# Kernel tuning notes

Measured on AMD Instinct MI355X. Metric: run time of the kernel, lower is better.

Reference implementation:

```python
import jax, jax.numpy as jnp
import numpy as np
from jax.scipy.linalg import expm

B, T, N_IN, N_HID, N_OUT = 8192, 2048, 2, 10, 10


def setup_inputs() -> dict:
    key = jax.random.key(0)
    k0, k1, k2, k3, k4 = jax.random.split(key, 5)
    inputs = jax.random.normal(k0, (B, T, N_IN), dtype=jnp.float32)
    # skew-symmetric seed for the orthogonal recurrent kernel (expm parametrization)
    A = jax.random.normal(k1, (N_HID, N_HID), dtype=jnp.float32) * 0.1
    # input_kernel: nn.Linear(n_inputs, n_hidden, bias=False) -> weight [H, D_in]
    W_in = jax.random.normal(k2, (N_HID, N_IN), dtype=jnp.float32) / np.sqrt(N_IN)
    # modrelu bias, initialized uniform(-0.01, 0.01) as in exprnn
    b_mod = jax.random.uniform(k3, (N_HID,), jnp.float32, -0.01, 0.01)
    # final nn.Linear(n_hidden, n_outputs)
    lin_W = jax.random.normal(k4, (N_OUT, N_HID), dtype=jnp.float32) / np.sqrt(N_HID)
    lin_b = jnp.zeros((N_OUT,), jnp.float32)
    return {"inputs": inputs, "A": A, "W_in": W_in, "b_mod": b_mod,
            "lin_W": lin_W, "lin_b": lin_b}


def _modrelu(z, b):
    # modrelu(z) = sign(z) * relu(|z| + b)
    return jnp.sign(z) * jax.nn.relu(jnp.abs(z) + b)


def reference(inputs, A, W_in, b_mod, lin_W, lin_b):
    # Orthogonal recurrent matrix: Bmat = expm(skew(A)), skew from strict upper triangle
    A_tri = jnp.triu(A, k=1)
    Bmat = expm(A_tri - A_tri.T)  # [H, H], orthogonal
    # Precompute input projections for all timesteps: [B, T, H]
    x_proj = jnp.einsum('btd,hd->bth', inputs, W_in)
    h0 = jnp.zeros((inputs.shape[0], W_in.shape[0]), dtype=inputs.dtype)

    def step(h, x_t):
        h_new = _modrelu(x_t + h @ Bmat, b_mod)
        return h_new, None

    hT, _ = jax.lax.scan(step, h0, jnp.swapaxes(x_proj, 0, 1))  # scan over time
    out = hT @ lin_W.T + lin_b  # [B, n_outputs]
    return out
```

## Files before the change

### kernel.cpp

```cpp
#include <hip/hip_runtime.h>
#include <hip/hip_bf16.h>

#define H 10
#define HP 16
#define T_LEN 2048
#define BATCH 8192

typedef _Float16 h4_t __attribute__((ext_vector_type(4)));
typedef __fp16   p2_t __attribute__((ext_vector_type(2)));
typedef float    f4_t __attribute__((ext_vector_type(4)));

__global__ void expm_kernel(const float* __restrict__ A, float* __restrict__ Bout) {
    __shared__ double S[H][H];
    __shared__ double P[H][H];
    __shared__ double E[H][H];
    const int tid = threadIdx.x;
    const int i = tid / H, j = tid % H;
    if (tid < H * H) {
        double a = 0.0;
        if (i < j) a = (double)A[i * H + j];
        else if (i > j) a = -(double)A[j * H + i];
        a *= (1.0 / 256.0);
        S[i][j] = a;
        P[i][j] = a;
        E[i][j] = (i == j ? 1.0 : 0.0) + a;
    }
    __syncthreads();
    for (int k = 2; k <= 16; ++k) {
        double acc = 0.0;
        if (tid < H * H) {
            for (int m = 0; m < H; ++m) acc += P[i][m] * S[m][j];
            acc *= (1.0 / (double)k);
        }
        __syncthreads();
        if (tid < H * H) { P[i][j] = acc; E[i][j] += acc; }
        __syncthreads();
    }
    for (int rr = 0; rr < 8; ++rr) {
        double acc = 0.0;
        if (tid < H * H) {
            for (int m = 0; m < H; ++m) acc += E[i][m] * E[m][j];
        }
        __syncthreads();
        if (tid < H * H) E[i][j] = acc;
        __syncthreads();
    }
    for (int idx = tid; idx < HP * HP; idx += blockDim.x) {
        const int i2 = idx / HP, j2 = idx % HP;
        Bout[idx] = (i2 < H && j2 < H) ? (float)E[i2][j2] : 0.0f;
    }
}

__global__ __launch_bounds__(64)
void rnn_kernel(const float* __restrict__ x,
                const float* __restrict__ Bp,
                const float* __restrict__ Win,
                const float* __restrict__ bmod,
                const float* __restrict__ lW,
                const float* __restrict__ lb,
                float* __restrict__ out) {
    const int l = threadIdx.x;
    const int m = l & 15;
    const int q = l >> 4;
    const int n0 = q * 4;
    const int batch = blockIdx.x * 16 + m;

    h4_t a_hi, a_lo;
    f4_t w0v, w1v, bmv;
#pragma unroll
    for (int i = 0; i < 4; ++i) {
        const float bv = Bp[(n0 + i) * HP + m];
        const _Float16 hi = (_Float16)bv;
        a_hi[i] = hi;
        a_lo[i] = (_Float16)(bv - (float)hi);
        const int n = n0 + i;
        w0v[i] = (n < H) ? Win[n * 2 + 0] : 0.0f;
        w1v[i] = (n < H) ? Win[n * 2 + 1] : 0.0f;
        bmv[i] = (n < H) ? bmod[n] : 0.0f;
    }

    float hs0 = 0.0f, hs1 = 0.0f, hs2 = 0.0f, hs3 = 0.0f;
    h4_t b_hi = {0, 0, 0, 0};
    h4_t b_lo = {0, 0, 0, 0};

    const float4* __restrict__ xp4 =
        (const float4*)(x + (size_t)batch * (T_LEN * 2));

    float4 buf0 = xp4[0], buf1 = xp4[1], buf2 = xp4[2], buf3 = xp4[3];

    for (int t0 = 0; t0 < T_LEN; t0 += 8) {
        const float4 c0 = buf0, c1 = buf1, c2 = buf2, c3 = buf3;
        if (t0 + 8 < T_LEN) {
            const int base = (t0 + 8) >> 1;
            buf0 = xp4[base + 0];
            buf1 = xp4[base + 1];
            buf2 = xp4[base + 2];
            buf3 = xp4[base + 3];
        }
        float xs[16];
        xs[0] = c0.x; xs[1] = c0.y; xs[2]  = c0.z; xs[3]  = c0.w;
        xs[4] = c1.x; xs[5] = c1.y; xs[6]  = c1.z; xs[7]  = c1.w;
        xs[8] = c2.x; xs[9] = c2.y; xs[10] = c2.z; xs[11] = c2.w;
        xs[12] = c3.x; xs[13] = c3.y; xs[14] = c3.z; xs[15] = c3.w;

#pragma unroll
        for (int u = 0; u < 8; ++u) {
            const float x0 = xs[2 * u], x1 = xs[2 * u + 1];
            f4_t c;
            c[0] = fmaf(x1, w1v[0], x0 * w0v[0]);
            c[1] = fmaf(x1, w1v[1], x0 * w0v[1]);
            c[2] = fmaf(x1, w1v[2], x0 * w0v[2]);
            c[3] = fmaf(x1, w1v[3], x0 * w0v[3]);

            f4_t acc = __builtin_amdgcn_mfma_f32_16x16x16f16(a_hi, b_hi, c, 0, 0, 0);
            acc = __builtin_amdgcn_mfma_f32_16x16x16f16(a_hi, b_lo, acc, 0, 0, 0);
            acc = __builtin_amdgcn_mfma_f32_16x16x16f16(a_lo, b_hi, acc, 0, 0, 0);

            const float z0 = acc[0], z1 = acc[1], z2 = acc[2], z3 = acc[3];
            hs0 = __builtin_copysignf(fmaxf(fabsf(z0) + bmv[0], 0.0f), z0);
            hs1 = __builtin_copysignf(fmaxf(fabsf(z1) + bmv[1], 0.0f), z1);
            hs2 = __builtin_copysignf(fmaxf(fabsf(z2) + bmv[2], 0.0f), z2);
            hs3 = __builtin_copysignf(fmaxf(fabsf(z3) + bmv[3], 0.0f), z3);

            const p2_t hi01 = __builtin_amdgcn_cvt_pkrtz(hs0, hs1);
            const p2_t hi23 = __builtin_amdgcn_cvt_pkrtz(hs2, hs3);
            const float l0 = hs0 - (float)hi01[0];
            const float l1 = hs1 - (float)hi01[1];
            const float l2 = hs2 - (float)hi23[0];
            const float l3 = hs3 - (float)hi23[1];
            const p2_t lo01 = __builtin_amdgcn_cvt_pkrtz(l0, l1);
            const p2_t lo23 = __builtin_amdgcn_cvt_pkrtz(l2, l3);
            b_hi[0] = (_Float16)hi01[0]; b_hi[1] = (_Float16)hi01[1];
            b_hi[2] = (_Float16)hi23[0]; b_hi[3] = (_Float16)hi23[1];
            b_lo[0] = (_Float16)lo01[0]; b_lo[1] = (_Float16)lo01[1];
            b_lo[2] = (_Float16)lo23[0]; b_lo[3] = (_Float16)lo23[1];
        }
    }

    __shared__ float hsh[16][17];
    hsh[m][n0 + 0] = hs0;
    hsh[m][n0 + 1] = hs1;
    hsh[m][n0 + 2] = hs2;
    hsh[m][n0 + 3] = hs3;
    __syncthreads();
#pragma unroll
    for (int jo = 0; jo < 3; ++jo) {
        const int o = q + 4 * jo;
        if (o < H) {
            float acc = lb[o];
#pragma unroll
            for (int jj = 0; jj < H; ++jj)
                acc = fmaf(hsh[m][jj], lW[o * H + jj], acc);
            out[(size_t)batch * H + o] = acc;
        }
    }
}

extern "C" void kernel_launch(void* const* d_in, const int* in_sizes, int n_in,
                              void* d_out, int out_size, void* d_ws, size_t ws_size,
                              hipStream_t stream) {
    const float* inputs = (const float*)d_in[0];
    const float* A      = (const float*)d_in[1];
    const float* W_in   = (const float*)d_in[2];
    const float* b_mod  = (const float*)d_in[3];
    const float* lin_W  = (const float*)d_in[4];
    const float* lin_b  = (const float*)d_in[5];
    float* out = (float*)d_out;
    float* Bpad = (float*)d_ws;

    expm_kernel<<<1, 128, 0, stream>>>(A, Bpad);
    rnn_kernel<<<BATCH / 16, 64, 0, stream>>>(inputs, Bpad, W_in, b_mod,
                                              lin_W, lin_b, out);
}
```

Baseline: 379.3 us.

## Drop hidden-state low-part MFMA and run correction MFMA in parallel

```diff
diff --git a/kernel.cpp b/kernel.cpp
--- a/kernel.cpp
+++ b/kernel.cpp
@@ -7,7 +7,6 @@
 #define BATCH 8192
 
 typedef _Float16 h4_t __attribute__((ext_vector_type(4)));
-typedef __fp16   p2_t __attribute__((ext_vector_type(2)));
 typedef float    f4_t __attribute__((ext_vector_type(4)));
 
 __global__ void expm_kernel(const float* __restrict__ A, float* __restrict__ Bout) {
@@ -81,28 +80,18 @@
 
     float hs0 = 0.0f, hs1 = 0.0f, hs2 = 0.0f, hs3 = 0.0f;
     h4_t b_hi = {0, 0, 0, 0};
-    h4_t b_lo = {0, 0, 0, 0};
+    const f4_t zero4 = {0.0f, 0.0f, 0.0f, 0.0f};
 
     const float4* __restrict__ xp4 =
         (const float4*)(x + (size_t)batch * (T_LEN * 2));
 
-    float4 buf0 = xp4[0], buf1 = xp4[1], buf2 = xp4[2], buf3 = xp4[3];
-
-    for (int t0 = 0; t0 < T_LEN; t0 += 8) {
-        const float4 c0 = buf0, c1 = buf1, c2 = buf2, c3 = buf3;
-        if (t0 + 8 < T_LEN) {
-            const int base = (t0 + 8) >> 1;
-            buf0 = xp4[base + 0];
-            buf1 = xp4[base + 1];
-            buf2 = xp4[base + 2];
-            buf3 = xp4[base + 3];
-        }
+    auto step8 = [&](const float4& c0, const float4& c1,
+                     const float4& c2, const float4& c3) {
         float xs[16];
         xs[0] = c0.x; xs[1] = c0.y; xs[2]  = c0.z; xs[3]  = c0.w;
         xs[4] = c1.x; xs[5] = c1.y; xs[6]  = c1.z; xs[7]  = c1.w;
         xs[8] = c2.x; xs[9] = c2.y; xs[10] = c2.z; xs[11] = c2.w;
         xs[12] = c3.x; xs[13] = c3.y; xs[14] = c3.z; xs[15] = c3.w;
-
 #pragma unroll
         for (int u = 0; u < 8; ++u) {
             const float x0 = xs[2 * u], x1 = xs[2 * u + 1];
@@ -112,29 +101,45 @@
             c[2] = fmaf(x1, w1v[2], x0 * w0v[2]);
             c[3] = fmaf(x1, w1v[3], x0 * w0v[3]);
 
-            f4_t acc = __builtin_amdgcn_mfma_f32_16x16x16f16(a_hi, b_hi, c, 0, 0, 0);
-            acc = __builtin_amdgcn_mfma_f32_16x16x16f16(a_hi, b_lo, acc, 0, 0, 0);
-            acc = __builtin_amdgcn_mfma_f32_16x16x16f16(a_lo, b_hi, acc, 0, 0, 0);
+            const f4_t m1 = __builtin_amdgcn_mfma_f32_16x16x16f16(a_hi, b_hi, c,     0, 0, 0);
+            const f4_t m2 = __builtin_amdgcn_mfma_f32_16x16x16f16(a_lo, b_hi, zero4, 0, 0, 0);
 
-            const float z0 = acc[0], z1 = acc[1], z2 = acc[2], z3 = acc[3];
+            const float z0 = m1[0] + m2[0];
+            const float z1 = m1[1] + m2[1];
+            const float z2 = m1[2] + m2[2];
+            const float z3 = m1[3] + m2[3];
+
             hs0 = __builtin_copysignf(fmaxf(fabsf(z0) + bmv[0], 0.0f), z0);
             hs1 = __builtin_copysignf(fmaxf(fabsf(z1) + bmv[1], 0.0f), z1);
             hs2 = __builtin_copysignf(fmaxf(fabsf(z2) + bmv[2], 0.0f), z2);
             hs3 = __builtin_copysignf(fmaxf(fabsf(z3) + bmv[3], 0.0f), z3);
 
-            const p2_t hi01 = __builtin_amdgcn_cvt_pkrtz(hs0, hs1);
-            const p2_t hi23 = __builtin_amdgcn_cvt_pkrtz(hs2, hs3);
-            const float l0 = hs0 - (float)hi01[0];
-            const float l1 = hs1 - (float)hi01[1];
-            const float l2 = hs2 - (float)hi23[0];
-            const float l3 = hs3 - (float)hi23[1];
-            const p2_t lo01 = __builtin_amdgcn_cvt_pkrtz(l0, l1);
-            const p2_t lo23 = __builtin_amdgcn_cvt_pkrtz(l2, l3);
-            b_hi[0] = (_Float16)hi01[0]; b_hi[1] = (_Float16)hi01[1];
-            b_hi[2] = (_Float16)hi23[0]; b_hi[3] = (_Float16)hi23[1];
-            b_lo[0] = (_Float16)lo01[0]; b_lo[1] = (_Float16)lo01[1];
-            b_lo[2] = (_Float16)lo23[0]; b_lo[3] = (_Float16)lo23[1];
+            b_hi[0] = (_Float16)hs0;
+            b_hi[1] = (_Float16)hs1;
+            b_hi[2] = (_Float16)hs2;
+            b_hi[3] = (_Float16)hs3;
         }
+    };
+
+    float4 a0 = xp4[0], a1 = xp4[1], a2 = xp4[2], a3 = xp4[3];
+    float4 b0 = xp4[4], b1 = xp4[5], b2 = xp4[6], b3 = xp4[7];
+
+    for (int t0 = 0; t0 < T_LEN; t0 += 16) {
+        const float4 ca0 = a0, ca1 = a1, ca2 = a2, ca3 = a3;
+        if (t0 + 16 < T_LEN) {
+            const int base = (t0 + 16) >> 1;
+            a0 = xp4[base + 0]; a1 = xp4[base + 1];
+            a2 = xp4[base + 2]; a3 = xp4[base + 3];
+        }
+        step8(ca0, ca1, ca2, ca3);
+
+        const float4 cb0 = b0, cb1 = b1, cb2 = b2, cb3 = b3;
+        if (t0 + 24 < T_LEN) {
+            const int base = (t0 + 24) >> 1;
+            b0 = xp4[base + 0]; b1 = xp4[base + 1];
+            b2 = xp4[base + 2]; b3 = xp4[base + 3];
+        }
+        step8(cb0, cb1, cb2, cb3);
     }
 
     __shared__ float hsh[16][17];
```

Result: slower. 423.5 us (+11.7%).
